# Kernel tuning notes

Measured on AMD Instinct MI355X. Metric: run time of the kernel, lower is better.

The kernel has to match this reference:

```python
import jax, jax.numpy as jnp
import numpy as np

NUM_ITERATIONS = 3
EPS = 1e-12  # matches torch F.normalize default eps


def setup_inputs() -> dict:
    key = jax.random.key(0)
    k1, k2 = jax.random.split(key)
    B, IN_CAPS, IN_LEN = 64, 1152, 8
    OUT_CAPS, OUT_LEN = 64, 16
    x = jax.random.normal(k1, (B, IN_CAPS, IN_LEN), dtype=jnp.float32)
    # xavier_uniform over (out_caps, out_len, in_len): fan_in=in_len, fan_out=out_len
    limit = float(np.sqrt(6.0 / (IN_LEN + OUT_LEN)))
    weight = jax.random.uniform(k2, (OUT_CAPS, OUT_LEN, IN_LEN), dtype=jnp.float32,
                                minval=-limit, maxval=limit)
    return {"x": x, "weight": weight}


def reference(x, weight):
    # priors[b,o,n,l] = sum_i weight[o,l,i] * x[b,n,i]  -> [B, out_caps, in_caps, out_len]
    priors = jnp.einsum('oli,bni->bonl', weight, x)
    # k-means routing, similarity='dot', squash=False (module defaults)
    out = jnp.mean(priors, axis=-2, keepdims=True)  # [B, O, 1, L] initial centroid
    probs = None
    for _ in range(NUM_ITERATIONS):
        norm = jnp.linalg.norm(out, axis=-1, keepdims=True)
        out_n = out / jnp.maximum(norm, EPS)  # F.normalize(output, dim=-1)
        logits = jnp.sum(priors * out_n, axis=-1, keepdims=True)  # [B, O, N, 1]
        probs = jax.nn.softmax(logits, axis=-2)  # softmax over in_capsules
        out = jnp.sum(probs * priors, axis=-2, keepdims=True)  # [B, O, 1, L]
    # squash=False -> return raw centroid
    return out.squeeze(-2), probs.squeeze(-1)  # [B, O, L], [B, O, N]
```

## Files before the change

### kernel.cpp

```cpp
#include <hip/hip_runtime.h>
#include <math.h>


#define NCAPS 1152
#define ILEN  8
#define OCAPS 64
#define OLEN  16
#define T     512
#define NWAVE 8
#define TPW   9
#define NITER 3
#define OG    16
#define XT_PITCH 1156

typedef __attribute__((ext_vector_type(8))) short short8;
typedef __attribute__((ext_vector_type(4))) float f32x4;

__device__ __forceinline__ unsigned f2bf_u(float f) {
    unsigned u = __builtin_bit_cast(unsigned, f);
    return (u + 0x7FFFu + ((u >> 16) & 1u)) >> 16;
}
__device__ __forceinline__ unsigned pack2(float a, float b) {
    return f2bf_u(a) | (f2bf_u(b) << 16);
}
__device__ __forceinline__ float bf2f(unsigned h) {
    return __builtin_bit_cast(float, h << 16);
}
__device__ __forceinline__ short8 s8_from(unsigned a, unsigned b, unsigned c, unsigned d) {
    uint4 t = make_uint4(a, b, c, d);
    return __builtin_bit_cast(short8, t);
}

template<int CTRL>
__device__ __forceinline__ float dpp_mov0(float x) {
    int xi = __builtin_bit_cast(int, x);
    int r  = __builtin_amdgcn_update_dpp(0, xi, CTRL, 0xf, 0xf, true);
    return __builtin_bit_cast(float, r);
}
__device__ __forceinline__ float row16_sum(float v) {
    v += dpp_mov0<0x111>(v);
    v += dpp_mov0<0x112>(v);
    v += dpp_mov0<0x114>(v);
    v += dpp_mov0<0x118>(v);
    return v;
}

__global__ __launch_bounds__(T, 2) void caps_kernel(const float* __restrict__ x,
                                                    const float* __restrict__ w,
                                                    float* __restrict__ dout,
                                                    int probs_base) {
    const int tid  = threadIdx.x;
    const int lane = tid & 63;
    const int wid  = tid >> 6;
    const int l16  = lane & 15;
    const int quad = lane >> 4;
    const bool q0  = (quad == 0);
    const int b  = blockIdx.x >> 2;
    const int og = blockIdx.x & 3;

    __shared__ __align__(16) unsigned short xA[NCAPS][ILEN];
    __shared__ __align__(16) unsigned short xaugT[10 * XT_PITCH];
    __shared__ __align__(16) unsigned short Yl[OLEN][16];
    __shared__ __align__(16) float Wl[OLEN][OLEN][ILEN];
    __shared__ float Scmb[NWAVE][OLEN][17];
    __shared__ float ZL[OLEN];

    ((float4*)&Wl[0][0][0])[tid] = ((const float4*)(w + (size_t)og * OG * OLEN * ILEN))[tid];

    const float4* xs = (const float4*)(x + (size_t)b * NCAPS * ILEN);
    #pragma unroll
    for (int p = 0; p < 3; ++p) {
        const int row = p * T + tid;
        if (row < NCAPS) {
            float4 x0 = xs[row * 2], x1 = xs[row * 2 + 1];
            unsigned h0 = f2bf_u(x0.x), h1 = f2bf_u(x0.y), h2 = f2bf_u(x0.z), h3 = f2bf_u(x0.w);
            unsigned h4 = f2bf_u(x1.x), h5 = f2bf_u(x1.y), h6 = f2bf_u(x1.z), h7 = f2bf_u(x1.w);
            *(uint4*)&xA[row][0] = make_uint4(h0 | (h1 << 16), h2 | (h3 << 16),
                                              h4 | (h5 << 16), h6 | (h7 << 16));
            xaugT[0 * XT_PITCH + row] = (unsigned short)h0;
            xaugT[1 * XT_PITCH + row] = (unsigned short)h1;
            xaugT[2 * XT_PITCH + row] = (unsigned short)h2;
            xaugT[3 * XT_PITCH + row] = (unsigned short)h3;
            xaugT[4 * XT_PITCH + row] = (unsigned short)h4;
            xaugT[5 * XT_PITCH + row] = (unsigned short)h5;
            xaugT[6 * XT_PITCH + row] = (unsigned short)h6;
            xaugT[7 * XT_PITCH + row] = (unsigned short)h7;
            xaugT[8 * XT_PITCH + row] = 0x3F80;
        }
    }
    for (int idx = tid; idx < XT_PITCH; idx += T) xaugT[9 * XT_PITCH + idx] = 0;
    __syncthreads();

    const int jr = (l16 < 9) ? l16 : 9;
    const unsigned short* xTw = xaugT + jr * XT_PITCH + wid * (TPW * 16) + 4 * quad;
    const unsigned short* xAw = &xA[wid * (TPW * 16) + l16][0];

    const short8 zs = {0, 0, 0, 0, 0, 0, 0, 0};
    const f32x4  zc = {0.f, 0.f, 0.f, 0.f};

    unsigned st0[TPW], st1[TPW];

    #pragma unroll
    for (int it = 0; it <= NITER; ++it) {
        short8 bL = zs;
        if (it > 0 && q0) bL = *(const short8*)&Yl[l16][0];

        f32x4 sacc = zc;
        #pragma unroll
        for (int tt = 0; tt < TPW; ++tt) {
            uint2 t2 = *(const uint2*)(xTw + tt * 16);
            short8 bs = s8_from(t2.x, t2.y, 0u, 0u);

            short8 as;
            if (it == 0) {
                as = s8_from(0x3F803F80u, 0x3F803F80u, 0u, 0u);
            } else {
                short8 aL = q0 ? *(const short8*)(xAw + tt * 128) : zs;
                f32x4 d = __builtin_amdgcn_mfma_f32_16x16x32_bf16(aL, bL, zc, 0, 0, 0);
                float e0 = __expf(d[0]), e1 = __expf(d[1]);
                float e2 = __expf(d[2]), e3 = __expf(d[3]);
                unsigned p0 = pack2(e0, e1), p1 = pack2(e2, e3);
                if (it == NITER) { st0[tt] = p0; st1[tt] = p1; }
                as = s8_from(p0, p1, 0u, 0u);
            }
            sacc = __builtin_amdgcn_mfma_f32_16x16x32_bf16(as, bs, sacc, 0, 0, 0);
        }

        #pragma unroll
        for (int r = 0; r < 4; ++r) Scmb[wid][4 * quad + r][l16] = sacc[r];
        __syncthreads();

        if (tid < 256) {
            const int o = tid >> 4, l = tid & 15;
            float sv[9];
            #pragma unroll
            for (int i = 0; i < 9; ++i) {
                float t = Scmb[0][o][i];
                #pragma unroll
                for (int ww = 1; ww < NWAVE; ++ww) t += Scmb[ww][o][i];
                sv[i] = t;
            }
            const float zinv = 1.0f / sv[8];
            const float* wrow = &Wl[o][l][0];
            float outl = wrow[0] * sv[0];
            #pragma unroll
            for (int i = 1; i < ILEN; ++i) outl = fmaf(wrow[i], sv[i], outl);
            outl *= zinv;

            if (it < NITER) {
                float n2 = outl * outl;
                n2 += __shfl_xor(n2, 1);
                n2 += __shfl_xor(n2, 2);
                n2 += __shfl_xor(n2, 4);
                n2 += __shfl_xor(n2, 8);
                const float inv = 1.0f / fmaxf(sqrtf(n2), 1e-12f);
                const float oh = outl * inv;
                #pragma unroll
                for (int i = 0; i < ILEN; ++i) {
                    float t = row16_sum(wrow[i] * oh);
                    if (l == 15) Yl[o][i] = (unsigned short)f2bf_u(t);
                }
            } else {
                dout[(((size_t)(b * OCAPS + og * OG + o)) << 4) + l] = outl;
                if (l == 0) ZL[o] = zinv;
            }
        }
        __syncthreads();
    }

    {
        const float zi = ZL[l16];
        float* pb = dout + (size_t)probs_base
                  + (size_t)(b * OCAPS + og * OG + l16) * NCAPS
                  + wid * (TPW * 16) + 4 * quad;
        #pragma unroll
        for (int tt = 0; tt < TPW; ++tt) {
            unsigned p0 = st0[tt], p1 = st1[tt];
            pb[tt * 16 + 0] = bf2f(p0 & 0xFFFFu) * zi;
            pb[tt * 16 + 1] = bf2f(p0 >> 16) * zi;
            pb[tt * 16 + 2] = bf2f(p1 & 0xFFFFu) * zi;
            pb[tt * 16 + 3] = bf2f(p1 >> 16) * zi;
        }
    }
}

extern "C" void kernel_launch(void* const* d_in, const int* in_sizes, int n_in,
                              void* d_out, int out_size, void* d_ws, size_t ws_size,
                              hipStream_t stream) {
    const float* x = (const float*)d_in[0];
    const float* w = (const float*)d_in[1];
    float* out = (float*)d_out;
    const int Bv = in_sizes[0] / (NCAPS * ILEN);
    const int nblocks = Bv * (OCAPS / OG);
    const int probs_base = Bv * OCAPS * OLEN;
    caps_kernel<<<dim3(nblocks), dim3(T), 0, stream>>>(x, w, out, probs_base);
}
```

Measured before the change: 72.63 us.

## Halve block size and out-caps per block, stage probs in LDS for coalesced stores

Each block now has 256 threads and handles 8 output capsules instead of 16, so twice as many blocks run, each with 18 tiles per wave. The iteration-0 mean is computed directly from fp32 x via DPP wave reductions instead of an MFMA pass. Final exp values are staged in LDS and written out as coalesced float4 rows rather than strided scalar stores. Cross-lane reductions switch from shuffles to DPP all-sums. The aim is better occupancy, coalesced output and less work in the first pass, at the cost of redundant x loading across twice as many blocks.

```diff
diff --git a/kernel.cpp b/kernel.cpp
--- a/kernel.cpp
+++ b/kernel.cpp
@@ -6,12 +6,13 @@
 #define ILEN  8
 #define OCAPS 64
 #define OLEN  16
-#define T     512
-#define NWAVE 8
-#define TPW   9
+#define T     256
+#define NWAVE 4
+#define TPW   18
 #define NITER 3
-#define OG    16
+#define OG    8
 #define XT_PITCH 1156
+#define E_PITCH  1160
 
 typedef __attribute__((ext_vector_type(8))) short short8;
 typedef __attribute__((ext_vector_type(4))) float f32x4;
@@ -32,16 +33,25 @@
 }
 
 template<int CTRL>
-__device__ __forceinline__ float dpp_mov0(float x) {
+__device__ __forceinline__ float dpp_add(float x) {
     int xi = __builtin_bit_cast(int, x);
     int r  = __builtin_amdgcn_update_dpp(0, xi, CTRL, 0xf, 0xf, true);
-    return __builtin_bit_cast(float, r);
-}
-__device__ __forceinline__ float row16_sum(float v) {
-    v += dpp_mov0<0x111>(v);
-    v += dpp_mov0<0x112>(v);
-    v += dpp_mov0<0x114>(v);
-    v += dpp_mov0<0x118>(v);
+    return x + __builtin_bit_cast(float, r);
+}
+__device__ __forceinline__ float wave_sum63(float v) {
+    v = dpp_add<0x111>(v);
+    v = dpp_add<0x112>(v);
+    v = dpp_add<0x114>(v);
+    v = dpp_add<0x118>(v);
+    v = dpp_add<0x142>(v);
+    v = dpp_add<0x143>(v);
+    return v;
+}
+__device__ __forceinline__ float allsum16(float v) {
+    v = dpp_add<0xB1>(v);
+    v = dpp_add<0x4E>(v);
+    v = dpp_add<0x124>(v);
+    v = dpp_add<0x128>(v);
     return v;
 }
 
@@ -55,24 +65,30 @@
     const int l16  = lane & 15;
     const int quad = lane >> 4;
     const bool q0  = (quad == 0);
-    const int b  = blockIdx.x >> 2;
-    const int og = blockIdx.x & 3;
+    const int b  = blockIdx.x >> 3;
+    const int og = blockIdx.x & 7;
 
     __shared__ __align__(16) unsigned short xA[NCAPS][ILEN];
     __shared__ __align__(16) unsigned short xaugT[10 * XT_PITCH];
     __shared__ __align__(16) unsigned short Yl[OLEN][16];
-    __shared__ __align__(16) float Wl[OLEN][OLEN][ILEN];
-    __shared__ float Scmb[NWAVE][OLEN][17];
-    __shared__ float ZL[OLEN];
+    __shared__ __align__(16) float Wl[OG][OLEN][ILEN];
+    __shared__ __align__(16) float Scmb[NWAVE][OLEN][17];
+    __shared__ __align__(16) unsigned short eL[OG * E_PITCH];
+    __shared__ float ZL[OG];
 
     ((float4*)&Wl[0][0][0])[tid] = ((const float4*)(w + (size_t)og * OG * OLEN * ILEN))[tid];
-
+    if (tid < 128) ((unsigned*)&Yl[0][0])[tid] = 0;
+
+    float acc0 = 0.f, acc1 = 0.f, acc2 = 0.f, acc3 = 0.f;
+    float acc4 = 0.f, acc5 = 0.f, acc6 = 0.f, acc7 = 0.f;
     const float4* xs = (const float4*)(x + (size_t)b * NCAPS * ILEN);
     #pragma unroll
-    for (int p = 0; p < 3; ++p) {
+    for (int p = 0; p < 5; ++p) {
         const int row = p * T + tid;
         if (row < NCAPS) {
             float4 x0 = xs[row * 2], x1 = xs[row * 2 + 1];
+            acc0 += x0.x; acc1 += x0.y; acc2 += x0.z; acc3 += x0.w;
+            acc4 += x1.x; acc5 += x1.y; acc6 += x1.z; acc7 += x1.w;
             unsigned h0 = f2bf_u(x0.x), h1 = f2bf_u(x0.y), h2 = f2bf_u(x0.z), h3 = f2bf_u(x0.w);
             unsigned h4 = f2bf_u(x1.x), h5 = f2bf_u(x1.y), h6 = f2bf_u(x1.z), h7 = f2bf_u(x1.w);
             *(uint4*)&xA[row][0] = make_uint4(h0 | (h1 << 16), h2 | (h3 << 16),
@@ -89,56 +105,72 @@
         }
     }
     for (int idx = tid; idx < XT_PITCH; idx += T) xaugT[9 * XT_PITCH + idx] = 0;
+
+    acc0 = wave_sum63(acc0); acc1 = wave_sum63(acc1);
+    acc2 = wave_sum63(acc2); acc3 = wave_sum63(acc3);
+    acc4 = wave_sum63(acc4); acc5 = wave_sum63(acc5);
+    acc6 = wave_sum63(acc6); acc7 = wave_sum63(acc7);
+    if (lane == 63) {
+        Scmb[wid][0][0] = acc0; Scmb[wid][0][1] = acc1;
+        Scmb[wid][0][2] = acc2; Scmb[wid][0][3] = acc3;
+        Scmb[wid][0][4] = acc4; Scmb[wid][0][5] = acc5;
+        Scmb[wid][0][6] = acc6; Scmb[wid][0][7] = acc7;
+    }
     __syncthreads();
 
     const int jr = (l16 < 9) ? l16 : 9;
     const unsigned short* xTw = xaugT + jr * XT_PITCH + wid * (TPW * 16) + 4 * quad;
     const unsigned short* xAw = &xA[wid * (TPW * 16) + l16][0];
-
     const short8 zs = {0, 0, 0, 0, 0, 0, 0, 0};
     const f32x4  zc = {0.f, 0.f, 0.f, 0.f};
 
-    unsigned st0[TPW], st1[TPW];
-
     #pragma unroll
     for (int it = 0; it <= NITER; ++it) {
-        short8 bL = zs;
-        if (it > 0 && q0) bL = *(const short8*)&Yl[l16][0];
-
-        f32x4 sacc = zc;
-        #pragma unroll
-        for (int tt = 0; tt < TPW; ++tt) {
-            uint2 t2 = *(const uint2*)(xTw + tt * 16);
-            short8 bs = s8_from(t2.x, t2.y, 0u, 0u);
-
-            short8 as;
-            if (it == 0) {
-                as = s8_from(0x3F803F80u, 0x3F803F80u, 0u, 0u);
-            } else {
+        if (it > 0) {
+            short8 bL = q0 ? *(const short8*)&Yl[l16][0] : zs;
+            f32x4 sacc = zc;
+            #pragma unroll
+            for (int tt = 0; tt < TPW; ++tt) {
+                uint2 t2 = *(const uint2*)(xTw + tt * 16);
+                short8 bs = s8_from(t2.x, t2.y, 0u, 0u);
                 short8 aL = q0 ? *(const short8*)(xAw + tt * 128) : zs;
                 f32x4 d = __builtin_amdgcn_mfma_f32_16x16x32_bf16(aL, bL, zc, 0, 0, 0);
                 float e0 = __expf(d[0]), e1 = __expf(d[1]);
                 float e2 = __expf(d[2]), e3 = __expf(d[3]);
                 unsigned p0 = pack2(e0, e1), p1 = pack2(e2, e3);
-                if (it == NITER) { st0[tt] = p0; st1[tt] = p1; }
-                as = s8_from(p0, p1, 0u, 0u);
+                if (it == NITER && l16 < OG) {
+                    const int n0 = wid * (TPW * 16) + tt * 16 + 4 * quad;
+                    *(unsigned*)&eL[l16 * E_PITCH + n0]     = p0;
+                    *(unsigned*)&eL[l16 * E_PITCH + n0 + 2] = p1;
+                }
+                short8 as = s8_from(p0, p1, 0u, 0u);
+                sacc = __builtin_amdgcn_mfma_f32_16x16x32_bf16(as, bs, sacc, 0, 0, 0);
             }
-            sacc = __builtin_amdgcn_mfma_f32_16x16x32_bf16(as, bs, sacc, 0, 0, 0);
-        }
-
-        #pragma unroll
-        for (int r = 0; r < 4; ++r) Scmb[wid][4 * quad + r][l16] = sacc[r];
-        __syncthreads();
-
-        if (tid < 256) {
+            #pragma unroll
+            for (int r = 0; r < 4; ++r) Scmb[wid][4 * quad + r][l16] = sacc[r];
+            __syncthreads();
+        }
+
+        if (tid < 128) {
             const int o = tid >> 4, l = tid & 15;
             float sv[9];
-            #pragma unroll
-            for (int i = 0; i < 9; ++i) {
-                float t = Scmb[0][o][i];
+            if (it == 0) {
                 #pragma unroll
-                for (int ww = 1; ww < NWAVE; ++ww) t += Scmb[ww][o][i];
-                sv[i] = t;
+                for (int i = 0; i < 8; ++i) {
+                    float t = Scmb[0][0][i];
+                    #pragma unroll
+                    for (int ww = 1; ww < NWAVE; ++ww) t += Scmb[ww][0][i];
+                    sv[i] = t;
+                }
+                sv[8] = (float)NCAPS;
+            } else {
+                #pragma unroll
+                for (int i = 0; i < 9; ++i) {
+                    float t = Scmb[0][o][i];
+                    #pragma unroll
+                    for (int ww = 1; ww < NWAVE; ++ww) t += Scmb[ww][o][i];
+                    sv[i] = t;
+                }
             }
             const float zinv = 1.0f / sv[8];
             const float* wrow = &Wl[o][l][0];
@@ -148,38 +180,34 @@
             outl *= zinv;
 
             if (it < NITER) {
-                float n2 = outl * outl;
-                n2 += __shfl_xor(n2, 1);
-                n2 += __shfl_xor(n2, 2);
-                n2 += __shfl_xor(n2, 4);
-                n2 += __shfl_xor(n2, 8);
+                float n2 = allsum16(outl * outl);
                 const float inv = 1.0f / fmaxf(sqrtf(n2), 1e-12f);
                 const float oh = outl * inv;
                 #pragma unroll
                 for (int i = 0; i < ILEN; ++i) {
-                    float t = row16_sum(wrow[i] * oh);
-                    if (l == 15) Yl[o][i] = (unsigned short)f2bf_u(t);
+                    float yi = allsum16(wrow[i] * oh);
+                    if (l == i) Yl[o][i] = (unsigned short)f2bf_u(yi);
                 }
             } else {
-                dout[(((size_t)(b * OCAPS + og * OG + o)) << 4) + l] = outl;
+                dout[((size_t)(b * OCAPS + og * OG)) * OLEN + tid] = outl;
                 if (l == 0) ZL[o] = zinv;
             }
         }
         __syncthreads();
     }
 
-    {
-        const float zi = ZL[l16];
-        float* pb = dout + (size_t)probs_base
-                  + (size_t)(b * OCAPS + og * OG + l16) * NCAPS
-                  + wid * (TPW * 16) + 4 * quad;
-        #pragma unroll
-        for (int tt = 0; tt < TPW; ++tt) {
-            unsigned p0 = st0[tt], p1 = st1[tt];
-            pb[tt * 16 + 0] = bf2f(p0 & 0xFFFFu) * zi;
-            pb[tt * 16 + 1] = bf2f(p0 >> 16) * zi;
-            pb[tt * 16 + 2] = bf2f(p1 & 0xFFFFu) * zi;
-            pb[tt * 16 + 3] = bf2f(p1 >> 16) * zi;
+    #pragma unroll
+    for (int o = 0; o < OG; ++o) {
+        const float zi = ZL[o];
+        float* pp = dout + (size_t)probs_base + (size_t)(b * OCAPS + og * OG + o) * NCAPS;
+        for (int c = tid; c < NCAPS / 4; c += T) {
+            uint2 t = *(const uint2*)&eL[o * E_PITCH + 4 * c];
+            float4 v;
+            v.x = bf2f(t.x & 0xFFFFu) * zi;
+            v.y = bf2f(t.x >> 16) * zi;
+            v.z = bf2f(t.y & 0xFFFFu) * zi;
+            v.w = bf2f(t.y >> 16) * zi;
+            ((float4*)pp)[c] = v;
         }
     }
 }
```

Measured after the change: 77.76 us. +7.1%, slower.
